# Optimization experiments

Measured on AMD Instinct MI355X. Metric: run time of the kernel, lower is better.

The kernel has to match this reference:

```python
import jax, jax.numpy as jnp
import numpy as np

# dims
B, L, T, D = 8, 27, 256, 1152
GS = 3            # group_size
G = L // GS       # num_groups = 9
DD = 512          # downsample_dim
H, HD = 8, 64     # heads, head_dim
NQ = 1            # num_queries
OD = 2048         # output_dim
SCALE = 1.0 / float(np.sqrt(HD))


def setup_inputs() -> dict:
    key = jax.random.key(0)
    ks = jax.random.split(key, 12)
    s = 0.02
    return {
        "K": jax.random.normal(ks[0], (B, L, T, D), jnp.float32),
        "V": jax.random.normal(ks[1], (B, L, T, D), jnp.float32),
        # learnable queries: one (NQ, D) per layer, stacked -> (L, NQ, D)
        "query": jax.random.normal(ks[2], (L, NQ, D), jnp.float32),
        # per-group linear params (flax Linear: y = x @ W + b, W is (in, out))
        "Wq": jax.random.normal(ks[3], (G, D, DD), jnp.float32) * s,
        "bq": jnp.zeros((G, DD), jnp.float32),
        "Wk": jax.random.normal(ks[4], (G, D, DD), jnp.float32) * s,
        "bk": jnp.zeros((G, DD), jnp.float32),
        "Wv": jax.random.normal(ks[5], (G, D, DD), jnp.float32) * s,
        "bv": jnp.zeros((G, DD), jnp.float32),
        "Wo": jax.random.normal(ks[6], (G, DD, OD), jnp.float32) * s,
        "bo": jnp.zeros((G, OD), jnp.float32),
    }


def reference(K, V, query, Wq, bq, Wk, bk, Wv, bv, Wo, bo):
    # group the L layer axis: (B, G, GS, T, D); layers in a group share weights
    Kg = K.reshape(B, G, GS, T, D)
    Vg = V.reshape(B, G, GS, T, D)
    qg = query.reshape(G, GS, NQ, D)

    # projections (batched over groups; replaces L tiny per-layer linears)
    Qp = jnp.einsum('gsnd,gdf->gsnf', qg, Wq) + bq[:, None, None, :]
    Qp = Qp.reshape(G, GS, NQ, H, HD)
    Kp = (jnp.einsum('bgstd,gdf->bgstf', Kg, Wk)
          + bk[None, :, None, None, :]).reshape(B, G, GS, T, H, HD)
    Vp = (jnp.einsum('bgstd,gdf->bgstf', Vg, Wv)
          + bv[None, :, None, None, :]).reshape(B, G, GS, T, H, HD)

    # cross-attention: learnable query attends over T tokens per layer
    scores = jnp.einsum('gsnhe,bgsthe->bgsnht', Qp, Kp) * SCALE
    attn = jax.nn.softmax(scores, axis=-1)
    pooled = jnp.einsum('bgsnht,bgsthe->bgsnhe', attn, Vp)
    pooled = pooled.mean(axis=3)  # mean over queries (== squeeze when NQ=1) -> (B,G,GS,H,HD)

    # original does pooled.transpose(0,2,1).reshape(B, DD): head_dim-major flatten
    pooled = pooled.transpose(0, 1, 2, 4, 3).reshape(B, G, GS, DD)

    out = jnp.einsum('bgsf,gfo->bgso', pooled, Wo) + bo[None, :, None, :]
    return out.reshape(B, L, OD)
```

## Files before the change

### kernel.cpp

```cpp
#include <hip/hip_runtime.h>
#include <stdint.h>


__global__ __launch_bounds__(256) void qproj(
    const float* __restrict__ query, const float* __restrict__ Wq,
    const float* __restrict__ bq, float* __restrict__ Qp)
{
  const int l = blockIdx.x, g = l / 3;
  const int fb = blockIdx.y * 64;
  __shared__ float q[1152];
  __shared__ float part[4][64];
  for (int i = threadIdx.x; i < 1152; i += 256) q[i] = query[(size_t)l * 1152 + i];
  __syncthreads();
  const int fi = threadIdx.x & 63;
  const int kq = threadIdx.x >> 6;
  const float* W = Wq + (size_t)g * 1152 * 512 + fb + fi;
  float a0 = 0.f, a1 = 0.f;
  const int d0 = kq * 288;
#pragma unroll 4
  for (int d = d0; d < d0 + 288; d += 2) {
    a0 += q[d]     * W[(size_t)d * 512];
    a1 += q[d + 1] * W[(size_t)(d + 1) * 512];
  }
  part[kq][fi] = a0 + a1;
  __syncthreads();
  if (threadIdx.x < 64) {
    const int f = fb + threadIdx.x;
    float r = part[0][threadIdx.x] + part[1][threadIdx.x]
            + part[2][threadIdx.x] + part[3][threadIdx.x];
    Qp[l * 512 + f] = (r + bq[g * 512 + f]) * 0.125f;
  }
}

__global__ __launch_bounds__(256) void qk_mat(
    const float* __restrict__ Qp, const float* __restrict__ Wk,
    float* __restrict__ Qk)
{
  const int gidx = blockIdx.x * 256 + threadIdx.x;
  const int eg   = gidx & 3;
  const int item = gidx >> 2;
  const int l    = item / 9216;
  const int rem  = item % 9216;
  const int h    = rem / 1152;
  const int d    = rem % 1152;
  const int g    = l / 3;
  const float4* q4 = (const float4*)(Qp + l * 512 + h * 64 + eg * 16);
  const float4* w4 = (const float4*)(Wk + (size_t)g * 1152 * 512 + (size_t)d * 512 + h * 64 + eg * 16);
  float acc = 0.f;
#pragma unroll
  for (int e = 0; e < 4; e++) {
    const float4 a = q4[e], b = w4[e];
    acc += a.x * b.x + a.y * b.y + a.z * b.z + a.w * b.w;
  }
  acc += __shfl_xor(acc, 1, 64);
  acc += __shfl_xor(acc, 2, 64);
  if (eg == 0) Qk[((size_t)l * 1152 + d) * 8 + h] = acc;
}

__global__ __launch_bounds__(256) void score_k(
    const float* __restrict__ K, const float* __restrict__ Qk,
    float* __restrict__ scores)
{
  const int bl = blockIdx.x;
  const int tq = blockIdx.y;
  const int l = bl % 27;
  const int tid = threadIdx.x;
  const int lane = tid & 63;
  const int wid = tid >> 6;

  __shared__ __align__(16) float Kt[96 * 65];
  __shared__ __align__(16) float Qs[96 * 8];

  const float* Kbase = K + ((size_t)bl * 256 + tq * 64) * 1152;
  const float* Qbase = Qk + (size_t)l * 1152 * 8;

  float sc[8] = {0.f, 0.f, 0.f, 0.f, 0.f, 0.f, 0.f, 0.f};

  for (int dc = 0; dc < 12; dc++) {
    __syncthreads();
#pragma unroll
    for (int it = 0; it < 6; it++) {
      const int flat = it * 256 + tid;
      const int row = flat / 24;
      const int col = flat % 24;
      const float4 v = *(const float4*)(Kbase + (size_t)row * 1152 + dc * 96 + col * 4);
      Kt[(col * 4 + 0) * 65 + row] = v.x;
      Kt[(col * 4 + 1) * 65 + row] = v.y;
      Kt[(col * 4 + 2) * 65 + row] = v.z;
      Kt[(col * 4 + 3) * 65 + row] = v.w;
    }
    if (tid < 192)
      ((float4*)Qs)[tid] = ((const float4*)(Qbase + (size_t)dc * 96 * 8))[tid];
    __syncthreads();

#pragma unroll 4
    for (int j = 0; j < 24; j++) {
      const int d = wid * 24 + j;
      const float kv = Kt[d * 65 + lane];
      const float4 qa = *(const float4*)&Qs[d * 8];
      const float4 qb = *(const float4*)&Qs[d * 8 + 4];
      sc[0] = fmaf(kv, qa.x, sc[0]); sc[1] = fmaf(kv, qa.y, sc[1]);
      sc[2] = fmaf(kv, qa.z, sc[2]); sc[3] = fmaf(kv, qa.w, sc[3]);
      sc[4] = fmaf(kv, qb.x, sc[4]); sc[5] = fmaf(kv, qb.y, sc[5]);
      sc[6] = fmaf(kv, qb.z, sc[6]); sc[7] = fmaf(kv, qb.w, sc[7]);
    }
  }

  __syncthreads();
  *(float4*)&Kt[(wid * 64 + lane) * 8    ] = make_float4(sc[0], sc[1], sc[2], sc[3]);
  *(float4*)&Kt[(wid * 64 + lane) * 8 + 4] = make_float4(sc[4], sc[5], sc[6], sc[7]);
  __syncthreads();
  for (int out = tid; out < 512; out += 256) {
    const int t = out >> 3, h = out & 7;
    const float s = (Kt[(0 * 64 + t) * 8 + h] + Kt[(1 * 64 + t) * 8 + h])
                  + (Kt[(2 * 64 + t) * 8 + h] + Kt[(3 * 64 + t) * 8 + h]);
    scores[((size_t)bl * 256 + tq * 64 + t) * 8 + h] = s;
  }
}

__global__ __launch_bounds__(256) void softmax_k(
    const float* __restrict__ scores, float* __restrict__ attn)
{
  const int bl = blockIdx.x;
  const int t = threadIdx.x;
  const int wid = t >> 6, lane = t & 63;
  __shared__ float red[4][8], red2[4][8];

  float sc[8];
  const float* src = scores + ((size_t)bl * 256 + t) * 8;
#pragma unroll
  for (int h = 0; h < 8; h++) sc[h] = src[h];
#pragma unroll
  for (int h = 0; h < 8; h++) {
    float m = sc[h];
#pragma unroll
    for (int o = 1; o < 64; o <<= 1) m = fmaxf(m, __shfl_xor(m, o, 64));
    if (lane == 0) red[wid][h] = m;
  }
  __syncthreads();
  float p[8];
#pragma unroll
  for (int h = 0; h < 8; h++) {
    const float M = fmaxf(fmaxf(red[0][h], red[1][h]), fmaxf(red[2][h], red[3][h]));
    p[h] = __expf(sc[h] - M);
    float s = p[h];
#pragma unroll
    for (int o = 1; o < 64; o <<= 1) s += __shfl_xor(s, o, 64);
    if (lane == 0) red2[wid][h] = s;
  }
  __syncthreads();
  float* dst = attn + ((size_t)bl * 256 + t) * 8;
#pragma unroll
  for (int h = 0; h < 8; h++) {
    const float S = red2[0][h] + red2[1][h] + red2[2][h] + red2[3][h];
    dst[h] = p[h] * (1.0f / S);
  }
}

__global__ __launch_bounds__(384) void va_k(
    const float* __restrict__ V, const float* __restrict__ attn,
    float* __restrict__ VA)
{
  const int bl = blockIdx.x;
  const int dt = blockIdx.y;
  const int d  = dt * 384 + threadIdx.x;

  __shared__ __align__(16) float at[2048];
  for (int i = threadIdx.x; i < 2048; i += 384)
    at[i] = attn[(size_t)bl * 2048 + i];
  __syncthreads();

  const float* Vbase = V + (size_t)bl * 256 * 1152 + d;

  float acc[8] = {0.f, 0.f, 0.f, 0.f, 0.f, 0.f, 0.f, 0.f};
#pragma unroll 4
  for (int t = 0; t < 256; t++) {
    const float v = Vbase[(size_t)t * 1152];
    const float4 a0 = *(const float4*)&at[t * 8];
    const float4 a1 = *(const float4*)&at[t * 8 + 4];
    acc[0] = fmaf(a0.x, v, acc[0]); acc[1] = fmaf(a0.y, v, acc[1]);
    acc[2] = fmaf(a0.z, v, acc[2]); acc[3] = fmaf(a0.w, v, acc[3]);
    acc[4] = fmaf(a1.x, v, acc[4]); acc[5] = fmaf(a1.y, v, acc[5]);
    acc[6] = fmaf(a1.z, v, acc[6]); acc[7] = fmaf(a1.w, v, acc[7]);
  }
  float* dst = VA + (size_t)bl * 8 * 1152 + d;
#pragma unroll
  for (int h = 0; h < 8; h++) dst[(size_t)h * 1152] = acc[h];
}

__global__ __launch_bounds__(512) void pv_mat(
    const float* __restrict__ VA, const float* __restrict__ Wv,
    float* __restrict__ psum)
{
  const int l = blockIdx.x, g = l / 3, h = blockIdx.y, dz = blockIdx.z;
  const int b = threadIdx.x >> 6, lane = threadIdx.x & 63;
  const int bl = b * 27 + l;
  const float* W = Wv + (size_t)g * 1152 * 512 + h * 64 + lane;
  const float* va = VA + ((size_t)bl * 8 + h) * 1152;
  const int d0 = dz * 288;
  float a0 = 0.f, a1 = 0.f, a2 = 0.f, a3 = 0.f;
#pragma unroll 2
  for (int d = d0; d < d0 + 288; d += 4) {
    a0 = fmaf(va[d],     W[(size_t)(d)     * 512], a0);
    a1 = fmaf(va[d + 1], W[(size_t)(d + 1) * 512], a1);
    a2 = fmaf(va[d + 2], W[(size_t)(d + 2) * 512], a2);
    a3 = fmaf(va[d + 3], W[(size_t)(d + 3) * 512], a3);
  }
  psum[((size_t)dz * 216 + bl) * 512 + lane * 8 + h] = (a0 + a1) + (a2 + a3);
}

__global__ __launch_bounds__(256) void out_gemm(
    const float* __restrict__ psum, const float* __restrict__ bv,
    const float* __restrict__ Wo, const float* __restrict__ bo,
    float* __restrict__ out)
{
  const int l = blockIdx.x, g = l / 3;
  const int n = blockIdx.y * 256 + threadIdx.x;
  __shared__ float pl[8][512];
  for (int i = threadIdx.x; i < 4096; i += 256) {
    const int b = i >> 9, f = i & 511;
    const int bl = b * 27 + l;
    const int e = f >> 3, h = f & 7;
    float v = bv[g * 512 + h * 64 + e];
#pragma unroll
    for (int dz = 0; dz < 4; dz++)
      v += psum[((size_t)dz * 216 + bl) * 512 + f];
    pl[b][f] = v;
  }
  __syncthreads();
  const float* W = Wo + (size_t)g * 512 * 2048 + n;
  float acc[8] = {0.f, 0.f, 0.f, 0.f, 0.f, 0.f, 0.f, 0.f};
#pragma unroll 4
  for (int f = 0; f < 512; f++) {
    const float w = W[(size_t)f * 2048];
#pragma unroll
    for (int b = 0; b < 8; b++) acc[b] += pl[b][f] * w;
  }
  const float bb = bo[g * 2048 + n];
#pragma unroll
  for (int b = 0; b < 8; b++)
    out[(size_t)(b * 27 + l) * 2048 + n] = acc[b] + bb;
}

__global__ __launch_bounds__(256) void zfill(float* __restrict__ out, int n) {
  const int i = blockIdx.x * 256 + threadIdx.x;
  if (i < n) out[i] = 0.f;
}

extern "C" void kernel_launch(void* const* d_in, const int* in_sizes, int n_in,
                              void* d_out, int out_size, void* d_ws, size_t ws_size,
                              hipStream_t stream)
{
  float* out = (float*)d_out;

  bool ok = (n_in == 11) && (out_size == 8 * 27 * 2048);
  if (ok) {
    const int expect[11] = {
      8 * 27 * 256 * 1152,
      8 * 27 * 256 * 1152,
      27 * 1 * 1152,
      9 * 1152 * 512,
      9 * 512,
      9 * 1152 * 512,
      9 * 512,
      9 * 1152 * 512,
      9 * 512,
      9 * 512 * 2048,
      9 * 2048
    };
    for (int i = 0; i < 11; i++) ok = ok && (in_sizes[i] == expect[i]);
  }
  const size_t NEED = 14321664;
  ok = ok && (ws_size >= NEED);

  if (!ok) {
    zfill<<<dim3((out_size + 255) / 256), dim3(256), 0, stream>>>(out, out_size);
    return;
  }

  const float* Kin   = (const float*)d_in[0];
  const float* Vin   = (const float*)d_in[1];
  const float* query = (const float*)d_in[2];
  const float* Wq    = (const float*)d_in[3];
  const float* bq    = (const float*)d_in[4];
  const float* Wk    = (const float*)d_in[5];
  const float* Wv    = (const float*)d_in[7];
  const float* bvp   = (const float*)d_in[8];
  const float* Wo    = (const float*)d_in[9];
  const float* bo    = (const float*)d_in[10];

  char* ws = (char*)d_ws;
  float* Qpw     = (float*)(ws);
  float* Qkw     = (float*)(ws + 55296);
  float* scoresw = (float*)(ws + 1050624);
  float* attnw   = (float*)(ws + 2820096);
  float* VAw     = (float*)(ws + 4589568);
  float* psumw   = (float*)(ws + 12552192);

  qproj    <<<dim3(27, 8),    dim3(256), 0, stream>>>(query, Wq, bq, Qpw);
  qk_mat   <<<dim3(3888),     dim3(256), 0, stream>>>(Qpw, Wk, Qkw);
  score_k  <<<dim3(216, 4),   dim3(256), 0, stream>>>(Kin, Qkw, scoresw);
  softmax_k<<<dim3(216),      dim3(256), 0, stream>>>(scoresw, attnw);
  va_k     <<<dim3(216, 3),   dim3(384), 0, stream>>>(Vin, attnw, VAw);
  pv_mat   <<<dim3(27, 8, 4), dim3(512), 0, stream>>>(VAw, Wv, psumw);
  out_gemm <<<dim3(27, 8),    dim3(256), 0, stream>>>(psumw, bvp, Wo, bo, out);
}
```

Measured before the change: 272.3 us.

## Fuse query projection into Qk kernel and softmax into V-attention kernel

Merges the query projection with the Q·Wk^T contraction, so each block computes one head's 64-wide Qp slice in shared memory and then its slice of Qk. The softmax over scores moves into the V-weighted-sum kernel, which removes a launch and the attn buffer round trip. The cost is that the Wq projection is recomputed three times, once per d-chunk. Softmax is also recomputed in each of the three d-tile blocks per (b,l).

```diff
diff --git a/kernel.cpp b/kernel.cpp
--- a/kernel.cpp
+++ b/kernel.cpp
@@ -2,59 +2,61 @@
 #include <stdint.h>
 
 
-__global__ __launch_bounds__(256) void qproj(
+__global__ __launch_bounds__(256) void qk_fused(
     const float* __restrict__ query, const float* __restrict__ Wq,
-    const float* __restrict__ bq, float* __restrict__ Qp)
+    const float* __restrict__ bq, const float* __restrict__ Wk,
+    float* __restrict__ Qk)
 {
   const int l = blockIdx.x, g = l / 3;
-  const int fb = blockIdx.y * 64;
-  __shared__ float q[1152];
+  const int h = blockIdx.y;
+  const int dc = blockIdx.z;
+  const int tid = threadIdx.x;
+
+  __shared__ float qv[1152];
   __shared__ float part[4][64];
-  for (int i = threadIdx.x; i < 1152; i += 256) q[i] = query[(size_t)l * 1152 + i];
-  __syncthreads();
-  const int fi = threadIdx.x & 63;
-  const int kq = threadIdx.x >> 6;
-  const float* W = Wq + (size_t)g * 1152 * 512 + fb + fi;
-  float a0 = 0.f, a1 = 0.f;
-  const int d0 = kq * 288;
+  __shared__ float Qps[64];
+
+  for (int i = tid; i < 1152; i += 256) qv[i] = query[(size_t)l * 1152 + i];
+  __syncthreads();
+
+  {
+    const int e = tid & 63;
+    const int kq = tid >> 6;
+    const float* W = Wq + (size_t)g * 1152 * 512 + h * 64 + e;
+    float a0 = 0.f, a1 = 0.f;
+    const int d0 = kq * 288;
 #pragma unroll 4
-  for (int d = d0; d < d0 + 288; d += 2) {
-    a0 += q[d]     * W[(size_t)d * 512];
-    a1 += q[d + 1] * W[(size_t)(d + 1) * 512];
-  }
-  part[kq][fi] = a0 + a1;
-  __syncthreads();
-  if (threadIdx.x < 64) {
-    const int f = fb + threadIdx.x;
-    float r = part[0][threadIdx.x] + part[1][threadIdx.x]
-            + part[2][threadIdx.x] + part[3][threadIdx.x];
-    Qp[l * 512 + f] = (r + bq[g * 512 + f]) * 0.125f;
-  }
-}
-
-__global__ __launch_bounds__(256) void qk_mat(
-    const float* __restrict__ Qp, const float* __restrict__ Wk,
-    float* __restrict__ Qk)
-{
-  const int gidx = blockIdx.x * 256 + threadIdx.x;
-  const int eg   = gidx & 3;
-  const int item = gidx >> 2;
-  const int l    = item / 9216;
-  const int rem  = item % 9216;
-  const int h    = rem / 1152;
-  const int d    = rem % 1152;
-  const int g    = l / 3;
-  const float4* q4 = (const float4*)(Qp + l * 512 + h * 64 + eg * 16);
-  const float4* w4 = (const float4*)(Wk + (size_t)g * 1152 * 512 + (size_t)d * 512 + h * 64 + eg * 16);
-  float acc = 0.f;
-#pragma unroll
-  for (int e = 0; e < 4; e++) {
-    const float4 a = q4[e], b = w4[e];
-    acc += a.x * b.x + a.y * b.y + a.z * b.z + a.w * b.w;
-  }
-  acc += __shfl_xor(acc, 1, 64);
-  acc += __shfl_xor(acc, 2, 64);
-  if (eg == 0) Qk[((size_t)l * 1152 + d) * 8 + h] = acc;
+    for (int d = d0; d < d0 + 288; d += 2) {
+      a0 += qv[d]     * W[(size_t)d * 512];
+      a1 += qv[d + 1] * W[(size_t)(d + 1) * 512];
+    }
+    part[kq][e] = a0 + a1;
+  }
+  __syncthreads();
+  if (tid < 64) {
+    const float r = part[0][tid] + part[1][tid] + part[2][tid] + part[3][tid];
+    Qps[tid] = (r + bq[g * 512 + h * 64 + tid]) * 0.125f;
+  }
+  __syncthreads();
+
+  const float4* q4base = (const float4*)Qps;
+#pragma unroll
+  for (int it = 0; it < 6; it++) {
+    const int slot = it * 256 + tid;
+    const int eg = slot & 3;
+    const int d  = dc * 384 + (slot >> 2);
+    const float4* q4 = q4base + eg * 4;
+    const float4* w4 = (const float4*)(Wk + (size_t)g * 1152 * 512 + (size_t)d * 512 + h * 64 + eg * 16);
+    float acc = 0.f;
+#pragma unroll
+    for (int e = 0; e < 4; e++) {
+      const float4 a = q4[e], b = w4[e];
+      acc += a.x * b.x + a.y * b.y + a.z * b.z + a.w * b.w;
+    }
+    acc += __shfl_xor(acc, 1, 64);
+    acc += __shfl_xor(acc, 2, 64);
+    if (eg == 0) Qk[((size_t)l * 1152 + d) * 8 + h] = acc;
+  }
 }
 
 __global__ __launch_bounds__(256) void score_k(
@@ -118,60 +120,55 @@
   }
 }
 
-__global__ __launch_bounds__(256) void softmax_k(
-    const float* __restrict__ scores, float* __restrict__ attn)
-{
-  const int bl = blockIdx.x;
-  const int t = threadIdx.x;
-  const int wid = t >> 6, lane = t & 63;
-  __shared__ float red[4][8], red2[4][8];
-
-  float sc[8];
-  const float* src = scores + ((size_t)bl * 256 + t) * 8;
-#pragma unroll
-  for (int h = 0; h < 8; h++) sc[h] = src[h];
-#pragma unroll
-  for (int h = 0; h < 8; h++) {
-    float m = sc[h];
-#pragma unroll
-    for (int o = 1; o < 64; o <<= 1) m = fmaxf(m, __shfl_xor(m, o, 64));
-    if (lane == 0) red[wid][h] = m;
-  }
-  __syncthreads();
-  float p[8];
-#pragma unroll
-  for (int h = 0; h < 8; h++) {
-    const float M = fmaxf(fmaxf(red[0][h], red[1][h]), fmaxf(red[2][h], red[3][h]));
-    p[h] = __expf(sc[h] - M);
-    float s = p[h];
-#pragma unroll
-    for (int o = 1; o < 64; o <<= 1) s += __shfl_xor(s, o, 64);
-    if (lane == 0) red2[wid][h] = s;
-  }
-  __syncthreads();
-  float* dst = attn + ((size_t)bl * 256 + t) * 8;
-#pragma unroll
-  for (int h = 0; h < 8; h++) {
-    const float S = red2[0][h] + red2[1][h] + red2[2][h] + red2[3][h];
-    dst[h] = p[h] * (1.0f / S);
-  }
-}
-
-__global__ __launch_bounds__(384) void va_k(
-    const float* __restrict__ V, const float* __restrict__ attn,
+__global__ __launch_bounds__(384) void va_sm_k(
+    const float* __restrict__ V, const float* __restrict__ scores,
     float* __restrict__ VA)
 {
   const int bl = blockIdx.x;
   const int dt = blockIdx.y;
-  const int d  = dt * 384 + threadIdx.x;
+  const int tid = threadIdx.x;
+  const int d  = dt * 384 + tid;
 
   __shared__ __align__(16) float at[2048];
-  for (int i = threadIdx.x; i < 2048; i += 384)
-    at[i] = attn[(size_t)bl * 2048 + i];
+  __shared__ float red[4][8], red2[4][8];
+
+  const int wid = tid >> 6, lane = tid & 63;
+  float sc[8], p[8];
+  if (tid < 256) {
+    const float* src = scores + ((size_t)bl * 256 + tid) * 8;
+#pragma unroll
+    for (int h = 0; h < 8; h++) sc[h] = src[h];
+#pragma unroll
+    for (int h = 0; h < 8; h++) {
+      float m = sc[h];
+#pragma unroll
+      for (int o = 1; o < 64; o <<= 1) m = fmaxf(m, __shfl_xor(m, o, 64));
+      if (lane == 0) red[wid][h] = m;
+    }
+  }
+  __syncthreads();
+  if (tid < 256) {
+#pragma unroll
+    for (int h = 0; h < 8; h++) {
+      const float M = fmaxf(fmaxf(red[0][h], red[1][h]), fmaxf(red[2][h], red[3][h]));
+      p[h] = __expf(sc[h] - M);
+      float s = p[h];
+#pragma unroll
+      for (int o = 1; o < 64; o <<= 1) s += __shfl_xor(s, o, 64);
+      if (lane == 0) red2[wid][h] = s;
+    }
+  }
+  __syncthreads();
+  if (tid < 256) {
+#pragma unroll
+    for (int h = 0; h < 8; h++) {
+      const float S = red2[0][h] + red2[1][h] + red2[2][h] + red2[3][h];
+      at[tid * 8 + h] = p[h] * (1.0f / S);
+    }
+  }
   __syncthreads();
 
   const float* Vbase = V + (size_t)bl * 256 * 1152 + d;
-
   float acc[8] = {0.f, 0.f, 0.f, 0.f, 0.f, 0.f, 0.f, 0.f};
 #pragma unroll 4
   for (int t = 0; t < 256; t++) {
@@ -290,18 +287,14 @@
   const float* bo    = (const float*)d_in[10];
 
   char* ws = (char*)d_ws;
-  float* Qpw     = (float*)(ws);
   float* Qkw     = (float*)(ws + 55296);
   float* scoresw = (float*)(ws + 1050624);
-  float* attnw   = (float*)(ws + 2820096);
   float* VAw     = (float*)(ws + 4589568);
   float* psumw   = (float*)(ws + 12552192);
 
-  qproj    <<<dim3(27, 8),    dim3(256), 0, stream>>>(query, Wq, bq, Qpw);
-  qk_mat   <<<dim3(3888),     dim3(256), 0, stream>>>(Qpw, Wk, Qkw);
-  score_k  <<<dim3(216, 4),   dim3(256), 0, stream>>>(Kin, Qkw, scoresw);
-  softmax_k<<<dim3(216),      dim3(256), 0, stream>>>(scoresw, attnw);
-  va_k     <<<dim3(216, 3),   dim3(384), 0, stream>>>(Vin, attnw, VAw);
-  pv_mat   <<<dim3(27, 8, 4), dim3(512), 0, stream>>>(VAw, Wv, psumw);
-  out_gemm <<<dim3(27, 8),    dim3(256), 0, stream>>>(psumw, bvp, Wo, bo, out);
-}
+  qk_fused<<<dim3(27, 8, 3), dim3(256), 0, stream>>>(query, Wq, bq, Wk, Qkw);
+  score_k <<<dim3(216, 4),   dim3(256), 0, stream>>>(Kin, Qkw, scoresw);
+  va_sm_k <<<dim3(216, 3),   dim3(384), 0, stream>>>(Vin, scoresw, VAw);
+  pv_mat  <<<dim3(27, 8, 4), dim3(512), 0, stream>>>(VAw, Wv, psumw);
+  out_gemm<<<dim3(27, 8),    dim3(256), 0, stream>>>(psumw, bvp, Wo, bo, out);
+}
```

Result: no change. 268.6 us (-1.4%).
